# Optimization experiments

Measured on AMD Instinct MI355X. Metric: run time of the kernel, lower is better.

Reference implementation:

```python
import jax, jax.numpy as jnp
import numpy as np

HARDLIM_THRESH = 0.2


def setup_inputs() -> dict:
    key = jax.random.key(0)
    k_inp, k_w1, k_b1, k_w2, k_b2 = jax.random.split(key, 5)
    B, D, H, F = 16384, 4096, 2048, 512
    scale1 = 1.0 / np.sqrt(D)
    scale2 = 1.0 / np.sqrt(H)
    return {
        "inp": jax.random.normal(k_inp, (B, D), dtype=jnp.float32),
        "W1": jax.random.normal(k_w1, (H, D), dtype=jnp.float32) * scale1,
        "b1": jax.random.normal(k_b1, (H,), dtype=jnp.float32) * scale1,
        "W2": jax.random.normal(k_w2, (F, H), dtype=jnp.float32) * scale2,
        "b2": jax.random.normal(k_b2, (F,), dtype=jnp.float32) * scale2,
        "k": 8,
    }


def reference(inp, W1, b1, W2, b2, k):
    # Linear -> ReLU -> Linear
    h = jax.nn.relu(inp @ W1.T + b1)            # [B, H]
    logits = h @ W2.T + b2                      # [B, F]
    # 'hard' attention: sigmoid -> keep top-k (zero the rest) -> hardlim(0.2)
    s = jax.nn.sigmoid(logits)
    topk_vals, _ = jax.lax.top_k(s, k)          # [B, k]
    kth = topk_vals[:, -1:]                     # per-row k-th largest value
    gated = jnp.where(s >= kth, s, 0.0)         # GetTopK: zero non-top-k entries
    out = jnp.where(gated > HARDLIM_THRESH, 1.0, 0.0).astype(inp.dtype)
    return out
```

## Files before the change

kernel.cpp:

```cpp
#include <hip/hip_runtime.h>
#include <math.h>
#include <type_traits>


#define BM 128
#define BN 128
#define BK 16

#define TAU   1.0e-4f
#define L02F -1.3862943611198906f

typedef __attribute__((ext_vector_type(8))) short  bf16x8;
typedef __attribute__((ext_vector_type(8))) ushort u16x8;
typedef __attribute__((ext_vector_type(4))) float  f32x4;

__device__ inline ushort bfhi(float f)   { return (ushort)(__float_as_uint(f) >> 16); }
__device__ inline float  bfhif(float f)  { return __uint_as_float(__float_as_uint(f) & 0xFFFF0000u); }

__device__ inline void gload_lds16(const void* g, void* l) {
    __builtin_amdgcn_global_load_lds(
        (const __attribute__((address_space(1))) unsigned int*)g,
        (__attribute__((address_space(3))) unsigned int*)l, 16, 0, 0);
}

__global__ __launch_bounds__(256) void split_kernel(
    const float* __restrict__ src, ushort* __restrict__ hi,
    ushort* __restrict__ lo, size_t n4)
{
    size_t i = (size_t)blockIdx.x * 256 + threadIdx.x;
    size_t stride = (size_t)gridDim.x * 256;
    for (; i < n4; i += stride) {
        float4 v = ((const float4*)src)[i];
        ushort4 h, l;
        h.x = bfhi(v.x); l.x = bfhi(v.x - bfhif(v.x));
        h.y = bfhi(v.y); l.y = bfhi(v.y - bfhif(v.y));
        h.z = bfhi(v.z); l.z = bfhi(v.z - bfhif(v.z));
        h.w = bfhi(v.w); l.w = bfhi(v.w - bfhif(v.w));
        ((ushort4*)hi)[i] = h;
        ((ushort4*)lo)[i] = l;
    }
}

template<int OUT_SPLIT>
__global__ __launch_bounds__(512, 2) void bgemm_glds(
    const ushort* __restrict__ aH, const ushort* __restrict__ aL,
    const ushort* __restrict__ wH, const ushort* __restrict__ wL,
    const float* __restrict__ bias,
    ushort* __restrict__ Chi, ushort* __restrict__ Clo,
    float* __restrict__ C32,
    int N, int K, int nbm, int nbn)
{
    __shared__ ushort lds[73728];
    const int t    = threadIdx.x;
    const int lane = t & 63;
    const int wave = t >> 6;
    const int wr   = wave >> 1;
    const int wc   = wave & 1;
    const int l15  = lane & 15;
    const int l4   = lane >> 4;

    const int bid = blockIdx.x;
    const int xcd = bid & 7;
    const int j   = bid >> 3;
    const int bm  = xcd * (nbm >> 3) + j / nbn;
    const int bn  = j % nbn;

    const int c   = lane & 3;
    const int rA0 = (wave * 2 + 0) * 16 + (lane >> 2);
    const int rA1 = (wave * 2 + 1) * 16 + (lane >> 2);
    const int rB  = wave * 16 + (lane >> 2);
    const size_t offA0 = (size_t)(bm * 256 + rA0) * K + (size_t)((c ^ ((rA0 >> 1) & 3)) * 8);
    const size_t offA1 = (size_t)(bm * 256 + rA1) * K + (size_t)((c ^ ((rA1 >> 1) & 3)) * 8);
    const size_t offB  = (size_t)(bn * 128 + rB ) * K + (size_t)((c ^ ((rB  >> 1) & 3)) * 8);
    const ushort* sAh0 = aH + offA0; const ushort* sAl0 = aL + offA0;
    const ushort* sAh1 = aH + offA1; const ushort* sAl1 = aL + offA1;
    const ushort* sBh  = wH + offB;  const ushort* sBl  = wL + offB;

    f32x4 acc[4][4];
    #pragma unroll
    for (int mi = 0; mi < 4; ++mi)
        #pragma unroll
        for (int ni = 0; ni < 4; ++ni)
            acc[mi][ni] = (f32x4){0.f, 0.f, 0.f, 0.f};

    auto stage = [&](int b, int kt) {
        const size_t ko = (size_t)kt * 32;
        ushort* L0 = &lds[b * 24576];
        gload_lds16(sAh0 + ko, L0 + (wave * 2 + 0) * 512);
        gload_lds16(sAh1 + ko, L0 + (wave * 2 + 1) * 512);
        gload_lds16(sAl0 + ko, L0 + 8192 + (wave * 2 + 0) * 512);
        gload_lds16(sAl1 + ko, L0 + 8192 + (wave * 2 + 1) * 512);
        gload_lds16(sBh + ko,  L0 + 16384 + wave * 512);
        gload_lds16(sBl + ko,  L0 + 20480 + wave * 512);
    };
    auto frag_read = [&](int b, bf16x8 ah[4], bf16x8 al[4], bf16x8 bh[4], bf16x8 bl[4]) {
        const ushort* L0 = &lds[b * 24576];
        #pragma unroll
        for (int mi = 0; mi < 4; ++mi) {
            int row = wr * 64 + mi * 16 + l15;
            int o = row * 32 + ((l4 ^ ((row >> 1) & 3)) << 3);
            ah[mi] = *(const bf16x8*)&L0[o];
            al[mi] = *(const bf16x8*)&L0[8192 + o];
        }
        #pragma unroll
        for (int ni = 0; ni < 4; ++ni) {
            int row = wc * 64 + ni * 16 + l15;
            int o = row * 32 + ((l4 ^ ((row >> 1) & 3)) << 3);
            bh[ni] = *(const bf16x8*)&L0[16384 + o];
            bl[ni] = *(const bf16x8*)&L0[20480 + o];
        }
    };
    auto do_mfma = [&](bf16x8 ah[4], bf16x8 al[4], bf16x8 bh[4], bf16x8 bl[4]) {
        __builtin_amdgcn_s_setprio(1);
        #pragma unroll
        for (int mi = 0; mi < 4; ++mi)
            #pragma unroll
            for (int ni = 0; ni < 4; ++ni) {
                acc[mi][ni] = __builtin_amdgcn_mfma_f32_16x16x32_bf16(ah[mi], bh[ni], acc[mi][ni], 0, 0, 0);
                acc[mi][ni] = __builtin_amdgcn_mfma_f32_16x16x32_bf16(ah[mi], bl[ni], acc[mi][ni], 0, 0, 0);
                acc[mi][ni] = __builtin_amdgcn_mfma_f32_16x16x32_bf16(al[mi], bh[ni], acc[mi][ni], 0, 0, 0);
            }
        __builtin_amdgcn_s_setprio(0);
    };

    stage(0, 0);
    stage(1, 1);
    asm volatile("s_waitcnt vmcnt(6)");
    __builtin_amdgcn_s_barrier();

    const int nt = K / 32;
    bf16x8 ah[4], al[4], bh[4], bl[4];

    for (int kt = 0; kt < nt - 2; ++kt) {
        frag_read(kt % 3, ah, al, bh, bl);
        stage((kt + 2) % 3, kt + 2);
        __builtin_amdgcn_sched_barrier(0);
        do_mfma(ah, al, bh, bl);
        asm volatile("s_waitcnt vmcnt(6)");
        asm volatile("s_waitcnt lgkmcnt(0)\n\ts_barrier" ::: "memory");
    }
    {
        frag_read((nt - 2) % 3, ah, al, bh, bl);
        do_mfma(ah, al, bh, bl);
        asm volatile("s_waitcnt vmcnt(0)");
        asm volatile("s_waitcnt lgkmcnt(0)\n\ts_barrier" ::: "memory");
    }
    {
        frag_read((nt - 1) % 3, ah, al, bh, bl);
        do_mfma(ah, al, bh, bl);
    }

    #pragma unroll
    for (int ni = 0; ni < 4; ++ni) {
        int col = bn * 128 + wc * 64 + ni * 16 + l15;
        float bv = bias[col];
        #pragma unroll
        for (int mi = 0; mi < 4; ++mi) {
            int rowb = bm * 256 + wr * 64 + mi * 16 + l4 * 4;
            #pragma unroll
            for (int r = 0; r < 4; ++r) {
                float v = acc[mi][ni][r] + bv;
                size_t idx = (size_t)(rowb + r) * N + col;
                if (OUT_SPLIT) {
                    v = fmaxf(v, 0.0f);
                    Chi[idx] = bfhi(v);
                    Clo[idx] = bfhi(v - bfhif(v));
                } else {
                    C32[idx] = v;
                }
            }
        }
    }
}

__global__ __launch_bounds__(512, 2) void bgemm1_8p(
    const float* __restrict__ inp,
    const ushort* __restrict__ w1h, const ushort* __restrict__ w1l,
    const float* __restrict__ b1,
    ushort* __restrict__ Chi, ushort* __restrict__ Clo)
{
    __shared__ ushort lds[73728];
    const int t    = threadIdx.x;
    const int lane = t & 63;
    const int wave = t >> 6;
    const int wr   = wave >> 1;
    const int wc   = wave & 1;
    const int l15  = lane & 15;
    const int l4   = lane >> 4;

    const int bid = blockIdx.x;
    const int xcd = bid & 7;
    const int j   = bid >> 3;
    const int bm  = xcd * 8 + (j >> 4);
    const int bn  = j & 15;

    const int ra  = t >> 1;
    const int kh  = t & 1;
    const int rb  = t >> 2;
    const int kqb = (t & 3) ^ ((rb >> 1) & 3);

    const float*  Abase = inp + ((size_t)(bm * 256 + ra)) * 4096 + kh * 16;
    const ushort* Bsh   = w1h + ((size_t)(bn * 128 + rb)) * 4096 + kqb * 8;
    const ushort* Bsl   = w1l + ((size_t)(bn * 128 + rb)) * 4096 + kqb * 8;

    f32x4 acc[4][4];
    #pragma unroll
    for (int mi = 0; mi < 4; ++mi)
        #pragma unroll
        for (int ni = 0; ni < 4; ++ni)
            acc[mi][ni] = (f32x4){0.f, 0.f, 0.f, 0.f};

    auto a_write = [&](int b, const f32x4 av[4]) {
        ushort h[16], l[16];
        #pragma unroll
        for (int i = 0; i < 4; ++i) {
            #pragma unroll
            for (int jj = 0; jj < 4; ++jj) {
                float x = av[i][jj];
                h[i * 4 + jj] = bfhi(x);
                l[i * 4 + jj] = bfhi(x - bfhif(x));
            }
        }
        ushort* A0 = &lds[b * 24576 + ra * 32];
        #pragma unroll
        for (int jj = 0; jj < 2; ++jj) {
            int u = (((2 * kh + jj) ^ ((ra >> 1) & 3)) << 3);
            *(u16x8*)&A0[u]        = *(const u16x8*)&h[jj * 8];
            *(u16x8*)&A0[8192 + u] = *(const u16x8*)&l[jj * 8];
        }
    };
    auto w_issue = [&](int b, int kt) {
        gload_lds16(Bsh + (size_t)kt * 32, &lds[b * 24576 + 16384 + wave * 512]);
        gload_lds16(Bsl + (size_t)kt * 32, &lds[b * 24576 + 20480 + wave * 512]);
    };
    auto a_load_asm = [&](int kt, f32x4 av[4]) {
        const float* p = Abase + (size_t)kt * 32;
        asm volatile("global_load_dwordx4 %0, %1, off"           : "=v"(av[0]) : "v"(p));
        asm volatile("global_load_dwordx4 %0, %1, off offset:16" : "=v"(av[1]) : "v"(p));
        asm volatile("global_load_dwordx4 %0, %1, off offset:32" : "=v"(av[2]) : "v"(p));
        asm volatile("global_load_dwordx4 %0, %1, off offset:48" : "=v"(av[3]) : "v"(p));
    };
    auto frag_read = [&](int b, bf16x8 ah[4], bf16x8 al[4], bf16x8 bh[4], bf16x8 bl[4]) {
        const ushort* L0 = &lds[b * 24576];
        #pragma unroll
        for (int mi = 0; mi < 4; ++mi) {
            int row = wr * 64 + mi * 16 + l15;
            int o = row * 32 + ((l4 ^ ((row >> 1) & 3)) << 3);
            ah[mi] = *(const bf16x8*)&L0[o];
            al[mi] = *(const bf16x8*)&L0[8192 + o];
        }
        #pragma unroll
        for (int ni = 0; ni < 4; ++ni) {
            int row = wc * 64 + ni * 16 + l15;
            int o = row * 32 + ((l4 ^ ((row >> 1) & 3)) << 3);
            bh[ni] = *(const bf16x8*)&L0[16384 + o];
            bl[ni] = *(const bf16x8*)&L0[20480 + o];
        }
    };
    auto do_mfma = [&](bf16x8 ah[4], bf16x8 al[4], bf16x8 bh[4], bf16x8 bl[4]) {
        __builtin_amdgcn_s_setprio(1);
        #pragma unroll
        for (int mi = 0; mi < 4; ++mi)
            #pragma unroll
            for (int ni = 0; ni < 4; ++ni) {
                acc[mi][ni] = __builtin_amdgcn_mfma_f32_16x16x32_bf16(ah[mi], bh[ni], acc[mi][ni], 0, 0, 0);
                acc[mi][ni] = __builtin_amdgcn_mfma_f32_16x16x32_bf16(ah[mi], bl[ni], acc[mi][ni], 0, 0, 0);
                acc[mi][ni] = __builtin_amdgcn_mfma_f32_16x16x32_bf16(al[mi], bh[ni], acc[mi][ni], 0, 0, 0);
            }
        __builtin_amdgcn_s_setprio(0);
    };
    #define BAR_KEEP() asm volatile("s_waitcnt lgkmcnt(0)\n\ts_barrier" ::: "memory")

    f32x4 avA[4], avB[4];
    {
        f32x4 a0[4];
        #pragma unroll
        for (int i = 0; i < 4; ++i) a0[i] = *(const f32x4*)(Abase + i * 4);
        a_write(0, a0);
        w_issue(0, 0);
        a_load_asm(1, avA);
        __builtin_amdgcn_sched_barrier(0);
        w_issue(1, 1);
        __builtin_amdgcn_sched_barrier(0);
        asm volatile("s_waitcnt vmcnt(6)");
        BAR_KEEP();
    }

    const int nt = 128;
    auto tile_body = [&](int kt, f32x4 (&cons)[4], f32x4 (&prod)[4]) {
        const int cur = kt % 3, nb1 = (kt + 1) % 3, nb2 = (kt + 2) % 3;
        bf16x8 ah[4], al[4], bh[4], bl[4];
        frag_read(cur, ah, al, bh, bl);
        a_load_asm(kt + 2, prod);
        __builtin_amdgcn_sched_barrier(0);
        w_issue(nb2, kt + 2);
        __builtin_amdgcn_sched_barrier(0);
        asm volatile("s_waitcnt vmcnt(6)");
        asm volatile("" : "+v"(cons[0]), "+v"(cons[1]), "+v"(cons[2]), "+v"(cons[3]));
        __builtin_amdgcn_sched_barrier(0);
        a_write(nb1, cons);
        do_mfma(ah, al, bh, bl);
        BAR_KEEP();
    };

    for (int kt = 0; kt < nt - 2; kt += 2) {
        tile_body(kt,     avA, avB);
        tile_body(kt + 1, avB, avA);
    }
    {
        const int kt = nt - 2;
        bf16x8 ah[4], al[4], bh[4], bl[4];
        frag_read(kt % 3, ah, al, bh, bl);
        asm volatile("s_waitcnt vmcnt(0)");
        asm volatile("" : "+v"(avA[0]), "+v"(avA[1]), "+v"(avA[2]), "+v"(avA[3]));
        __builtin_amdgcn_sched_barrier(0);
        a_write((kt + 1) % 3, avA);
        do_mfma(ah, al, bh, bl);
        BAR_KEEP();
    }
    {
        bf16x8 ah[4], al[4], bh[4], bl[4];
        frag_read((nt - 1) % 3, ah, al, bh, bl);
        do_mfma(ah, al, bh, bl);
    }

    #pragma unroll
    for (int ni = 0; ni < 4; ++ni) {
        int col = bn * 128 + wc * 64 + ni * 16 + l15;
        float bv = b1[col];
        #pragma unroll
        for (int mi = 0; mi < 4; ++mi) {
            int rowb = bm * 256 + wr * 64 + mi * 16 + l4 * 4;
            #pragma unroll
            for (int r = 0; r < 4; ++r) {
                float v = fmaxf(acc[mi][ni][r] + bv, 0.0f);
                size_t idx = (size_t)(rowb + r) * 2048 + col;
                Chi[idx] = bfhi(v);
                Clo[idx] = bfhi(v - bfhif(v));
            }
        }
    }
    #undef BAR_KEEP
}

__global__ __launch_bounds__(256) void repair_r1(
    const float* __restrict__ inp,
    const float* __restrict__ W1, const float* __restrict__ b1,
    double* __restrict__ h64,
    const int* __restrict__ risky, const int* __restrict__ cnt, int maxr)
{
    int c = *cnt; if (c > maxr) c = maxr;
    const int by = blockIdx.y;
    if (by * 4 >= c) return;
    __shared__ float Xs[4][4096];
    const int t = threadIdx.x;

    int ridx[4];
    #pragma unroll
    for (int r = 0; r < 4; ++r) {
        int slot = by * 4 + r;
        ridx[r] = risky[slot < c ? slot : (c - 1)];
    }
    #pragma unroll
    for (int i = 0; i < 16; ++i) {
        int lin = t + i * 256;
        int r = lin >> 10, q = lin & 1023;
        *(float4*)&Xs[r][q * 4] = *(const float4*)(inp + (size_t)ridx[r] * 4096 + q * 4);
    }
    __syncthreads();

    const int n0 = blockIdx.x * 512 + t;
    const int n1 = n0 + 256;
    const float* w0 = W1 + (size_t)n0 * 4096;
    const float* w1 = W1 + (size_t)n1 * 4096;
    double acc[2][4] = {};

    for (int k = 0; k < 4096; k += 4) {
        float4 a0 = *(const float4*)(w0 + k);
        float4 a1 = *(const float4*)(w1 + k);
        float xr[4][4];
        #pragma unroll
        for (int r = 0; r < 4; ++r)
            *(float4*)&xr[r][0] = *(const float4*)&Xs[r][k];
        const float* ap0 = &a0.x;
        const float* ap1 = &a1.x;
        #pragma unroll
        for (int j = 0; j < 4; ++j) {
            double wd0 = (double)ap0[j];
            double wd1 = (double)ap1[j];
            #pragma unroll
            for (int r = 0; r < 4; ++r) {
                double xd = (double)xr[r][j];
                acc[0][r] = fma(wd0, xd, acc[0][r]);
                acc[1][r] = fma(wd1, xd, acc[1][r]);
            }
        }
    }

    double bv0 = (double)b1[n0], bv1 = (double)b1[n1];
    #pragma unroll
    for (int r = 0; r < 4; ++r) {
        int slot = by * 4 + r;
        if (slot < c) {
            h64[(size_t)slot * 2048 + n0] = fmax(acc[0][r] + bv0, 0.0);
            h64[(size_t)slot * 2048 + n1] = fmax(acc[1][r] + bv1, 0.0);
        }
    }
}

__global__ __launch_bounds__(256) void repair_r2(
    const double* __restrict__ h64,
    const float* __restrict__ W2, const float* __restrict__ b2,
    double* __restrict__ L64,
    const int* __restrict__ cnt, int maxr)
{
    int c = *cnt; if (c > maxr) c = maxr;
    const int by = blockIdx.y;
    if (by * 4 >= c) return;
    __shared__ double Xs[4][2048];
    const int t = threadIdx.x;

    #pragma unroll
    for (int i = 0; i < 16; ++i) {
        int lin = t + i * 256;
        int r = lin >> 10, q = lin & 1023;
        int slot = by * 4 + r; if (slot >= c) slot = c - 1;
        *(double2*)&Xs[r][q * 2] = *(const double2*)(h64 + (size_t)slot * 2048 + q * 2);
    }
    __syncthreads();

    const int n0 = t;
    const int n1 = t + 256;
    const float* w0 = W2 + (size_t)n0 * 2048;
    const float* w1 = W2 + (size_t)n1 * 2048;
    double acc[2][4] = {};

    for (int k = 0; k < 2048; k += 4) {
        float4 a0 = *(const float4*)(w0 + k);
        float4 a1 = *(const float4*)(w1 + k);
        double xr[4][4];
        #pragma unroll
        for (int r = 0; r < 4; ++r) {
            *(double2*)&xr[r][0] = *(const double2*)&Xs[r][k];
            *(double2*)&xr[r][2] = *(const double2*)&Xs[r][k + 2];
        }
        const float* ap0 = &a0.x;
        const float* ap1 = &a1.x;
        #pragma unroll
        for (int j = 0; j < 4; ++j) {
            double wd0 = (double)ap0[j];
            double wd1 = (double)ap1[j];
            #pragma unroll
            for (int r = 0; r < 4; ++r) {
                acc[0][r] = fma(wd0, xr[r][j], acc[0][r]);
                acc[1][r] = fma(wd1, xr[r][j], acc[1][r]);
            }
        }
    }

    double bv0 = (double)b2[n0], bv1 = (double)b2[n1];
    #pragma unroll
    for (int r = 0; r < 4; ++r) {
        int slot = by * 4 + r;
        if (slot < c) {
            L64[(size_t)slot * 512 + n0] = acc[0][r] + bv0;
            L64[(size_t)slot * 512 + n1] = acc[1][r] + bv1;
        }
    }
}

template<typename TA, int MODE>
__global__ __launch_bounds__(256, 1) void gemm64(
    const TA* __restrict__ A, int lda,
    const float* __restrict__ W, int ldw,
    const float* __restrict__ bias,
    double* __restrict__ out64, int N, int K)
{
    __shared__ double As[BK][BM + 2];
    __shared__ double Bs[BK][BN + 2];
    const int t  = threadIdx.x;
    const int tm = t >> 4;
    const int tn = t & 15;
    const size_t bm = blockIdx.x;
    const size_t bn = blockIdx.y;
    const TA*    Ab = A + bm * BM * (size_t)lda;
    const float* Wb = W + bn * BN * (size_t)ldw;

    double acc[8][8] = {};

    for (int k0 = 0; k0 < K; k0 += BK) {
        #pragma unroll
        for (int i = 0; i < 2; ++i) {
            int f   = t + i * 256;
            int row = f >> 2;
            int kc  = (f & 3) << 2;
            if constexpr (std::is_same<TA, double>::value) {
                double2 v0 = *(const double2*)(Ab + (size_t)row * lda + k0 + kc);
                double2 v1 = *(const double2*)(Ab + (size_t)row * lda + k0 + kc + 2);
                As[kc + 0][row] = v0.x; As[kc + 1][row] = v0.y;
                As[kc + 2][row] = v1.x; As[kc + 3][row] = v1.y;
            } else {
                float4 va = *(const float4*)(Ab + (size_t)row * lda + k0 + kc);
                As[kc + 0][row] = (double)va.x; As[kc + 1][row] = (double)va.y;
                As[kc + 2][row] = (double)va.z; As[kc + 3][row] = (double)va.w;
            }
            float4 vb = *(const float4*)(Wb + (size_t)row * ldw + k0 + kc);
            Bs[kc + 0][row] = (double)vb.x; Bs[kc + 1][row] = (double)vb.y;
            Bs[kc + 2][row] = (double)vb.z; Bs[kc + 3][row] = (double)vb.w;
        }
        __syncthreads();
        #pragma unroll
        for (int k = 0; k < BK; ++k) {
            double a[8], b[8];
            #pragma unroll
            for (int i = 0; i < 4; ++i) {
                *(double2*)&a[i * 2] = *(const double2*)&As[k][tm * 8 + i * 2];
                *(double2*)&b[i * 2] = *(const double2*)&Bs[k][tn * 8 + i * 2];
            }
            #pragma unroll
            for (int i = 0; i < 8; ++i)
                #pragma unroll
                for (int j = 0; j < 8; ++j)
                    acc[i][j] = fma(a[i], b[j], acc[i][j]);
        }
        __syncthreads();
    }

    double bv[8];
    if (MODE != 2) {
        #pragma unroll
        for (int j = 0; j < 8; ++j) bv[j] = (double)bias[bn * BN + tn * 8 + j];
    }

    #pragma unroll
    for (int i = 0; i < 8; ++i) {
        size_t row  = bm * BM + (size_t)tm * 8 + i;
        size_t base = row * (size_t)N + bn * BN + tn * 8;
        #pragma unroll
        for (int j = 0; j < 8; ++j) {
            double v = acc[i][j];
            if (MODE == 0) out64[base + j] = fmax(v + bv[j], 0.0);
            if (MODE == 1) out64[base + j] = v + bv[j];
            if (MODE == 2) out64[base + j] += v;
        }
    }
}

__global__ void init_repair(int* risky, int* cnt, int maxr)
{
    int i = blockIdx.x * 256 + threadIdx.x;
    if (i == 0) *cnt = 0;
    if (i < maxr) risky[i] = 0;
}

__global__ __launch_bounds__(256) void margin_topk32(
    const float* L, float* O, int ncols,
    const int* __restrict__ kp, int* __restrict__ risky, int* __restrict__ cnt,
    int maxr)
{
    const int wave = threadIdx.x >> 6;
    const int lane = threadIdx.x & 63;
    const int k = *kp;
    const size_t row = (size_t)blockIdx.x * 4 + wave;
    const float* Lr = L + row * (size_t)ncols;

    float v[8];
    *(float4*)&v[0] = *(const float4*)(Lr + lane * 8);
    *(float4*)&v[4] = *(const float4*)(Lr + lane * 8 + 4);
    float w[8];
    #pragma unroll
    for (int j = 0; j < 8; ++j) w[j] = v[j];

    float kth = -3.0e38f, minD = 3.0e38f;
    for (int it = 0; it < k; ++it) {
        float mv = w[0]; int mj = 0;
        #pragma unroll
        for (int j = 1; j < 8; ++j)
            if (w[j] > mv) { mv = w[j]; mj = j; }
        int mi = lane * 8 + mj;
        #pragma unroll
        for (int off = 32; off; off >>= 1) {
            float ov = __shfl_xor(mv, off);
            int   oi = __shfl_xor(mi, off);
            if (ov > mv || (ov == mv && oi < mi)) { mv = ov; mi = oi; }
        }
        kth = mv;
        minD = fminf(minD, fabsf(mv - L02F));
        if ((mi >> 3) == lane) w[mi & 7] = -3.0e38f;
    }
    float nv = w[0];
    #pragma unroll
    for (int j = 1; j < 8; ++j) nv = fmaxf(nv, w[j]);
    #pragma unroll
    for (int off = 32; off; off >>= 1) nv = fmaxf(nv, __shfl_xor(nv, off));

    bool risk = ((kth - nv) < 2.0f * TAU) || (minD < TAU);
    if (risk && lane == 0) {
        int p = atomicAdd(cnt, 1);
        if (p < maxr) risky[p] = (int)row;
    }

    float o[8];
    #pragma unroll
    for (int j = 0; j < 8; ++j)
        o[j] = (v[j] >= kth && v[j] > L02F) ? 1.0f : 0.0f;
    float* Op = O + row * (size_t)ncols + lane * 8;
    *(float4*)&Op[0] = *(const float4*)&o[0];
    *(float4*)&Op[4] = *(const float4*)&o[4];
}

__global__ __launch_bounds__(256) void topk64_kernel(
    const double* __restrict__ L, float* __restrict__ O, int ncols,
    const int* __restrict__ kp,
    const int* __restrict__ risky, const int* __restrict__ cnt, int maxr)
{
    const int wave = threadIdx.x >> 6;
    const int lane = threadIdx.x & 63;
    const int k = *kp;
    size_t pos = (size_t)blockIdx.x * 4 + wave;
    size_t row = pos;
    if (cnt) {
        int c = *cnt; if (c > maxr) c = maxr;
        if ((int)pos >= c) return;
        row = (size_t)risky[pos];
    }
    const double* Lr = L + pos * (size_t)ncols;

    double v[8];
    #pragma unroll
    for (int j = 0; j < 8; ++j) {
        double l = Lr[lane * 8 + j];
        v[j] = 1.0 / (1.0 + exp(-l));
    }
    double w[8];
    #pragma unroll
    for (int j = 0; j < 8; ++j) w[j] = v[j];

    double kth = -1.0e300;
    for (int it = 0; it < k; ++it) {
        double mv = w[0]; int mj = 0;
        #pragma unroll
        for (int j = 1; j < 8; ++j)
            if (w[j] > mv) { mv = w[j]; mj = j; }
        int mi = lane * 8 + mj;
        #pragma unroll
        for (int off = 32; off; off >>= 1) {
            double ov = __shfl_xor(mv, off);
            int    oi = __shfl_xor(mi, off);
            if (ov > mv || (ov == mv && oi < mi)) { mv = ov; mi = oi; }
        }
        kth = mv;
        if ((mi >> 3) == lane) w[mi & 7] = -1.0e300;
    }

    float o[8];
    #pragma unroll
    for (int j = 0; j < 8; ++j)
        o[j] = (v[j] >= kth && v[j] > 0.2) ? 1.0f : 0.0f;
    float* Op = O + row * (size_t)ncols + lane * 8;
    *(float4*)&Op[0] = *(const float4*)&o[0];
    *(float4*)&Op[4] = *(const float4*)&o[4];
}

extern "C" void kernel_launch(void* const* d_in, const int* in_sizes, int n_in,
                              void* d_out, int out_size, void* d_ws, size_t ws_size,
                              hipStream_t stream) {
    const float* inp = (const float*)d_in[0];
    const float* W1  = (const float*)d_in[1];
    const float* b1  = (const float*)d_in[2];
    const float* W2  = (const float*)d_in[3];
    const float* b2  = (const float*)d_in[4];
    const int*   kp  = (const int*)d_in[5];

    const int H = in_sizes[2];
    const int F = in_sizes[4];
    const int D = in_sizes[1] / H;
    const int B = in_sizes[0] / D;
    float* out = (float*)d_out;

    const int MAXR = 8192;
    const size_t szHpair = (size_t)B * H * 4;
    const size_t szW1p   = (size_t)H * D * 4;
    const size_t szW2p   = (size_t)F * H * 4;
    const size_t szInpP  = (size_t)B * D * 4;
    const size_t needMain = szHpair + szW1p + szW2p + (size_t)MAXR * 4 + 256;
    const size_t needA    = needMain + szInpP;
    const bool shapeOK = (D == 4096 && H == 2048 && F == 512 && B == 16384);

    if (shapeOK && ws_size >= needMain) {
        ushort* h_hi  = (ushort*)d_ws;
        ushort* h_lo  = h_hi + (size_t)B * H;
        ushort* w1h   = (ushort*)((char*)d_ws + szHpair);
        ushort* w1l   = w1h + (size_t)H * D;
        ushort* w2h   = (ushort*)((char*)d_ws + szHpair + szW1p);
        ushort* w2l   = w2h + (size_t)F * H;
        int*    risky = (int*)((char*)d_ws + szHpair + szW1p + szW2p);
        int*    cnt   = risky + MAXR;
        double* h64   = (double*)d_ws;
        double* L64   = (double*)((char*)d_ws + szHpair);
        float*  l32   = out;

        init_repair<<<(MAXR + 255) / 256, 256, 0, stream>>>(risky, cnt, MAXR);
        split_kernel<<<2048, 256, 0, stream>>>(W1, w1h, w1l, (size_t)H * D / 4);
        split_kernel<<<512, 256, 0, stream>>>(W2, w2h, w2l, (size_t)F * H / 4);

        if (ws_size >= needA) {
            ushort* inH = (ushort*)((char*)d_ws + needMain);
            ushort* inL = inH + (size_t)B * D;
            split_kernel<<<4096, 256, 0, stream>>>(inp, inH, inL, (size_t)B * D / 4);
            bgemm_glds<1><<<1024, 512, 0, stream>>>(
                inH, inL, w1h, w1l, b1, h_hi, h_lo, nullptr, H, D, B / 256, H / 128);
        } else {
            bgemm1_8p<<<1024, 512, 0, stream>>>(inp, w1h, w1l, b1, h_hi, h_lo);
        }
        bgemm_glds<0><<<256, 512, 0, stream>>>(
            h_hi, h_lo, w2h, w2l, b2, nullptr, nullptr, l32, F, H, B / 256, F / 128);

        margin_topk32<<<B / 4, 256, 0, stream>>>(l32, out, F, kp, risky, cnt, MAXR);
        repair_r1<<<dim3(4, MAXR / 4), 256, 0, stream>>>(
            inp, W1, b1, h64, risky, cnt, MAXR);
        repair_r2<<<dim3(1, MAXR / 4), 256, 0, stream>>>(
            h64, W2, b2, L64, cnt, MAXR);
        topk64_kernel<<<MAXR / 4, 256, 0, stream>>>(L64, out, F, kp, risky, cnt, MAXR);
    } else {
        int Hc = H, Bc = 0;
        for (;;) {
            size_t perRow = (size_t)F * 8 + (size_t)Hc * 8;
            Bc = (int)((ws_size / perRow) / BM) * BM;
            if (Bc >= BM || Hc <= BM) break;
            Hc >>= 1;
        }
        if (Bc < BM) Bc = BM;
        if (Bc > B)  Bc = B;
        double* L   = (double*)d_ws;
        double* h64 = L + (size_t)Bc * F;

        for (int b0 = 0; b0 < B; b0 += Bc) {
            int bc = (B - b0 < Bc) ? (B - b0) : Bc;
            for (int h0 = 0; h0 < H; h0 += Hc) {
                int hc = (H - h0 < Hc) ? (H - h0) : Hc;
                gemm64<float, 0><<<dim3(bc / BM, hc / BN), 256, 0, stream>>>(
                    inp + (size_t)b0 * D, D, W1 + (size_t)h0 * D, D, b1 + h0,
                    h64, hc, D);
                if (h0 == 0)
                    gemm64<double, 1><<<dim3(bc / BM, F / BN), 256, 0, stream>>>(
                        h64, hc, W2 + h0, H, b2, L, F, hc);
                else
                    gemm64<double, 2><<<dim3(bc / BM, F / BN), 256, 0, stream>>>(
                        h64, hc, W2 + h0, H, b2, L, F, hc);
            }
            topk64_kernel<<<bc / 4, 256, 0, stream>>>(
                L, out + (size_t)b0 * F, F, kp, nullptr, nullptr, 0);
        }
    }
}
```

Measured before the change: 1.402 ms.

## Use 256x256 tiled pre-split GEMM1, fold counter init, retile repair kernel

Replaces the first GEMM path with a new kernel that loads pre-split bf16 hi/lo operands through direct global-to-LDS loads into 256x256 tiles, double-buffered. Each tile gets more operand reuse and the grid needs fewer blocks. The init_repair launch is dropped and the counter reset moves into the first split kernel, which saves one launch. The repair_r1 kernel now handles 8 rows per block with one output column per thread. The code path now requires enough workspace for a split copy of the input and drops the fallback that split the input on the fly. The double-buffered loop waits on vmcnt(0) every iteration, which may expose load latency.

```diff
diff --git a/kernel.cpp b/kernel.cpp
--- a/kernel.cpp
+++ b/kernel.cpp
@@ -25,8 +25,9 @@
 
 __global__ __launch_bounds__(256) void split_kernel(
     const float* __restrict__ src, ushort* __restrict__ hi,
-    ushort* __restrict__ lo, size_t n4)
-{
+    ushort* __restrict__ lo, size_t n4, int* cnt)
+{
+    if (cnt && blockIdx.x == 0 && threadIdx.x == 0) *cnt = 0;
     size_t i = (size_t)blockIdx.x * 256 + threadIdx.x;
     size_t stride = (size_t)gridDim.x * 256;
     for (; i < n4; i += stride) {
@@ -38,6 +39,121 @@
         h.w = bfhi(v.w); l.w = bfhi(v.w - bfhif(v.w));
         ((ushort4*)hi)[i] = h;
         ((ushort4*)lo)[i] = l;
+    }
+}
+
+__global__ __launch_bounds__(512, 2) void bgemm1_256(
+    const ushort* __restrict__ aH, const ushort* __restrict__ aL,
+    const ushort* __restrict__ wH, const ushort* __restrict__ wL,
+    const float* __restrict__ b1,
+    ushort* __restrict__ Chi, ushort* __restrict__ Clo)
+{
+    __shared__ ushort lds[65536];
+    const int t    = threadIdx.x;
+    const int lane = t & 63;
+    const int wave = t >> 6;
+    const int wr   = wave >> 1;
+    const int wc   = wave & 1;
+    const int l15  = lane & 15;
+    const int l4   = lane >> 4;
+
+    const int bid = blockIdx.x;
+    const int xcd = bid & 7;
+    const int j   = bid >> 3;
+    const int bm  = xcd * 8 + (j >> 3);
+    const int bn  = j & 7;
+
+    const int cq = lane & 3;
+    const int r0 = wave * 32 + (lane >> 2);
+    const int r1 = r0 + 16;
+    const size_t sw0 = (size_t)((cq ^ ((r0 >> 1) & 3)) * 8);
+    const size_t sw1 = (size_t)((cq ^ ((r1 >> 1) & 3)) * 8);
+    const size_t gA0 = (size_t)(bm * 256 + r0) * 4096 + sw0;
+    const size_t gA1 = (size_t)(bm * 256 + r1) * 4096 + sw1;
+    const size_t gB0 = (size_t)(bn * 256 + r0) * 4096 + sw0;
+    const size_t gB1 = (size_t)(bn * 256 + r1) * 4096 + sw1;
+
+    f32x4 acc[4][8];
+    #pragma unroll
+    for (int mi = 0; mi < 4; ++mi)
+        #pragma unroll
+        for (int ni = 0; ni < 8; ++ni)
+            acc[mi][ni] = (f32x4){0.f, 0.f, 0.f, 0.f};
+
+    auto stage = [&](int b, int kt) {
+        const size_t ko = (size_t)kt * 32;
+        ushort* L0 = &lds[b * 32768];
+        gload_lds16(aH + gA0 + ko, L0 + wave * 1024);
+        gload_lds16(aH + gA1 + ko, L0 + wave * 1024 + 512);
+        gload_lds16(aL + gA0 + ko, L0 + 8192 + wave * 1024);
+        gload_lds16(aL + gA1 + ko, L0 + 8192 + wave * 1024 + 512);
+        gload_lds16(wH + gB0 + ko, L0 + 16384 + wave * 1024);
+        gload_lds16(wH + gB1 + ko, L0 + 16384 + wave * 1024 + 512);
+        gload_lds16(wL + gB0 + ko, L0 + 24576 + wave * 1024);
+        gload_lds16(wL + gB1 + ko, L0 + 24576 + wave * 1024 + 512);
+    };
+    auto compute = [&](int b) {
+        const ushort* L0 = &lds[b * 32768];
+        bf16x8 ah[4], al[4];
+        #pragma unroll
+        for (int mi = 0; mi < 4; ++mi) {
+            int row = wr * 64 + mi * 16 + l15;
+            int o = row * 32 + ((l4 ^ ((row >> 1) & 3)) << 3);
+            ah[mi] = *(const bf16x8*)&L0[o];
+            al[mi] = *(const bf16x8*)&L0[8192 + o];
+        }
+        #pragma unroll
+        for (int h = 0; h < 2; ++h) {
+            bf16x8 bh[4], bl[4];
+            #pragma unroll
+            for (int q = 0; q < 4; ++q) {
+                int row = wc * 128 + (h * 4 + q) * 16 + l15;
+                int o = row * 32 + ((l4 ^ ((row >> 1) & 3)) << 3);
+                bh[q] = *(const bf16x8*)&L0[16384 + o];
+                bl[q] = *(const bf16x8*)&L0[24576 + o];
+            }
+            __builtin_amdgcn_s_setprio(1);
+            #pragma unroll
+            for (int mi = 0; mi < 4; ++mi)
+                #pragma unroll
+                for (int q = 0; q < 4; ++q) {
+                    acc[mi][h * 4 + q] = __builtin_amdgcn_mfma_f32_16x16x32_bf16(ah[mi], bh[q], acc[mi][h * 4 + q], 0, 0, 0);
+                    acc[mi][h * 4 + q] = __builtin_amdgcn_mfma_f32_16x16x32_bf16(ah[mi], bl[q], acc[mi][h * 4 + q], 0, 0, 0);
+                    acc[mi][h * 4 + q] = __builtin_amdgcn_mfma_f32_16x16x32_bf16(al[mi], bh[q], acc[mi][h * 4 + q], 0, 0, 0);
+                }
+            __builtin_amdgcn_s_setprio(0);
+        }
+    };
+
+    stage(0, 0);
+    asm volatile("s_waitcnt vmcnt(0)");
+    __builtin_amdgcn_s_barrier();
+
+    const int nt = 128;
+    for (int kt = 0; kt < nt - 1; ++kt) {
+        stage((kt + 1) & 1, kt + 1);
+        __builtin_amdgcn_sched_barrier(0);
+        compute(kt & 1);
+        asm volatile("s_waitcnt vmcnt(0)");
+        asm volatile("s_waitcnt lgkmcnt(0)\n\ts_barrier" ::: "memory");
+    }
+    compute((nt - 1) & 1);
+
+    #pragma unroll
+    for (int ni = 0; ni < 8; ++ni) {
+        int col = bn * 256 + wc * 128 + ni * 16 + l15;
+        float bv = b1[col];
+        #pragma unroll
+        for (int mi = 0; mi < 4; ++mi) {
+            int rowb = bm * 256 + wr * 64 + mi * 16 + l4 * 4;
+            #pragma unroll
+            for (int r = 0; r < 4; ++r) {
+                float v = fmaxf(acc[mi][ni][r] + bv, 0.0f);
+                size_t idx = (size_t)(rowb + r) * 2048 + col;
+                Chi[idx] = bfhi(v);
+                Clo[idx] = bfhi(v - bfhif(v));
+            }
+        }
     }
 }
 
@@ -173,176 +289,6 @@
     }
 }
 
-__global__ __launch_bounds__(512, 2) void bgemm1_8p(
-    const float* __restrict__ inp,
-    const ushort* __restrict__ w1h, const ushort* __restrict__ w1l,
-    const float* __restrict__ b1,
-    ushort* __restrict__ Chi, ushort* __restrict__ Clo)
-{
-    __shared__ ushort lds[73728];
-    const int t    = threadIdx.x;
-    const int lane = t & 63;
-    const int wave = t >> 6;
-    const int wr   = wave >> 1;
-    const int wc   = wave & 1;
-    const int l15  = lane & 15;
-    const int l4   = lane >> 4;
-
-    const int bid = blockIdx.x;
-    const int xcd = bid & 7;
-    const int j   = bid >> 3;
-    const int bm  = xcd * 8 + (j >> 4);
-    const int bn  = j & 15;
-
-    const int ra  = t >> 1;
-    const int kh  = t & 1;
-    const int rb  = t >> 2;
-    const int kqb = (t & 3) ^ ((rb >> 1) & 3);
-
-    const float*  Abase = inp + ((size_t)(bm * 256 + ra)) * 4096 + kh * 16;
-    const ushort* Bsh   = w1h + ((size_t)(bn * 128 + rb)) * 4096 + kqb * 8;
-    const ushort* Bsl   = w1l + ((size_t)(bn * 128 + rb)) * 4096 + kqb * 8;
-
-    f32x4 acc[4][4];
-    #pragma unroll
-    for (int mi = 0; mi < 4; ++mi)
-        #pragma unroll
-        for (int ni = 0; ni < 4; ++ni)
-            acc[mi][ni] = (f32x4){0.f, 0.f, 0.f, 0.f};
-
-    auto a_write = [&](int b, const f32x4 av[4]) {
-        ushort h[16], l[16];
-        #pragma unroll
-        for (int i = 0; i < 4; ++i) {
-            #pragma unroll
-            for (int jj = 0; jj < 4; ++jj) {
-                float x = av[i][jj];
-                h[i * 4 + jj] = bfhi(x);
-                l[i * 4 + jj] = bfhi(x - bfhif(x));
-            }
-        }
-        ushort* A0 = &lds[b * 24576 + ra * 32];
-        #pragma unroll
-        for (int jj = 0; jj < 2; ++jj) {
-            int u = (((2 * kh + jj) ^ ((ra >> 1) & 3)) << 3);
-            *(u16x8*)&A0[u]        = *(const u16x8*)&h[jj * 8];
-            *(u16x8*)&A0[8192 + u] = *(const u16x8*)&l[jj * 8];
-        }
-    };
-    auto w_issue = [&](int b, int kt) {
-        gload_lds16(Bsh + (size_t)kt * 32, &lds[b * 24576 + 16384 + wave * 512]);
-        gload_lds16(Bsl + (size_t)kt * 32, &lds[b * 24576 + 20480 + wave * 512]);
-    };
-    auto a_load_asm = [&](int kt, f32x4 av[4]) {
-        const float* p = Abase + (size_t)kt * 32;
-        asm volatile("global_load_dwordx4 %0, %1, off"           : "=v"(av[0]) : "v"(p));
-        asm volatile("global_load_dwordx4 %0, %1, off offset:16" : "=v"(av[1]) : "v"(p));
-        asm volatile("global_load_dwordx4 %0, %1, off offset:32" : "=v"(av[2]) : "v"(p));
-        asm volatile("global_load_dwordx4 %0, %1, off offset:48" : "=v"(av[3]) : "v"(p));
-    };
-    auto frag_read = [&](int b, bf16x8 ah[4], bf16x8 al[4], bf16x8 bh[4], bf16x8 bl[4]) {
-        const ushort* L0 = &lds[b * 24576];
-        #pragma unroll
-        for (int mi = 0; mi < 4; ++mi) {
-            int row = wr * 64 + mi * 16 + l15;
-            int o = row * 32 + ((l4 ^ ((row >> 1) & 3)) << 3);
-            ah[mi] = *(const bf16x8*)&L0[o];
-            al[mi] = *(const bf16x8*)&L0[8192 + o];
-        }
-        #pragma unroll
-        for (int ni = 0; ni < 4; ++ni) {
-            int row = wc * 64 + ni * 16 + l15;
-            int o = row * 32 + ((l4 ^ ((row >> 1) & 3)) << 3);
-            bh[ni] = *(const bf16x8*)&L0[16384 + o];
-            bl[ni] = *(const bf16x8*)&L0[20480 + o];
-        }
-    };
-    auto do_mfma = [&](bf16x8 ah[4], bf16x8 al[4], bf16x8 bh[4], bf16x8 bl[4]) {
-        __builtin_amdgcn_s_setprio(1);
-        #pragma unroll
-        for (int mi = 0; mi < 4; ++mi)
-            #pragma unroll
-            for (int ni = 0; ni < 4; ++ni) {
-                acc[mi][ni] = __builtin_amdgcn_mfma_f32_16x16x32_bf16(ah[mi], bh[ni], acc[mi][ni], 0, 0, 0);
-                acc[mi][ni] = __builtin_amdgcn_mfma_f32_16x16x32_bf16(ah[mi], bl[ni], acc[mi][ni], 0, 0, 0);
-                acc[mi][ni] = __builtin_amdgcn_mfma_f32_16x16x32_bf16(al[mi], bh[ni], acc[mi][ni], 0, 0, 0);
-            }
-        __builtin_amdgcn_s_setprio(0);
-    };
-    #define BAR_KEEP() asm volatile("s_waitcnt lgkmcnt(0)\n\ts_barrier" ::: "memory")
-
-    f32x4 avA[4], avB[4];
-    {
-        f32x4 a0[4];
-        #pragma unroll
-        for (int i = 0; i < 4; ++i) a0[i] = *(const f32x4*)(Abase + i * 4);
-        a_write(0, a0);
-        w_issue(0, 0);
-        a_load_asm(1, avA);
-        __builtin_amdgcn_sched_barrier(0);
-        w_issue(1, 1);
-        __builtin_amdgcn_sched_barrier(0);
-        asm volatile("s_waitcnt vmcnt(6)");
-        BAR_KEEP();
-    }
-
-    const int nt = 128;
-    auto tile_body = [&](int kt, f32x4 (&cons)[4], f32x4 (&prod)[4]) {
-        const int cur = kt % 3, nb1 = (kt + 1) % 3, nb2 = (kt + 2) % 3;
-        bf16x8 ah[4], al[4], bh[4], bl[4];
-        frag_read(cur, ah, al, bh, bl);
-        a_load_asm(kt + 2, prod);
-        __builtin_amdgcn_sched_barrier(0);
-        w_issue(nb2, kt + 2);
-        __builtin_amdgcn_sched_barrier(0);
-        asm volatile("s_waitcnt vmcnt(6)");
-        asm volatile("" : "+v"(cons[0]), "+v"(cons[1]), "+v"(cons[2]), "+v"(cons[3]));
-        __builtin_amdgcn_sched_barrier(0);
-        a_write(nb1, cons);
-        do_mfma(ah, al, bh, bl);
-        BAR_KEEP();
-    };
-
-    for (int kt = 0; kt < nt - 2; kt += 2) {
-        tile_body(kt,     avA, avB);
-        tile_body(kt + 1, avB, avA);
-    }
-    {
-        const int kt = nt - 2;
-        bf16x8 ah[4], al[4], bh[4], bl[4];
-        frag_read(kt % 3, ah, al, bh, bl);
-        asm volatile("s_waitcnt vmcnt(0)");
-        asm volatile("" : "+v"(avA[0]), "+v"(avA[1]), "+v"(avA[2]), "+v"(avA[3]));
-        __builtin_amdgcn_sched_barrier(0);
-        a_write((kt + 1) % 3, avA);
-        do_mfma(ah, al, bh, bl);
-        BAR_KEEP();
-    }
-    {
-        bf16x8 ah[4], al[4], bh[4], bl[4];
-        frag_read((nt - 1) % 3, ah, al, bh, bl);
-        do_mfma(ah, al, bh, bl);
-    }
-
-    #pragma unroll
-    for (int ni = 0; ni < 4; ++ni) {
-        int col = bn * 128 + wc * 64 + ni * 16 + l15;
-        float bv = b1[col];
-        #pragma unroll
-        for (int mi = 0; mi < 4; ++mi) {
-            int rowb = bm * 256 + wr * 64 + mi * 16 + l4 * 4;
-            #pragma unroll
-            for (int r = 0; r < 4; ++r) {
-                float v = fmaxf(acc[mi][ni][r] + bv, 0.0f);
-                size_t idx = (size_t)(rowb + r) * 2048 + col;
-                Chi[idx] = bfhi(v);
-                Clo[idx] = bfhi(v - bfhif(v));
-            }
-        }
-    }
-    #undef BAR_KEEP
-}
-
 __global__ __launch_bounds__(256) void repair_r1(
     const float* __restrict__ inp,
     const float* __restrict__ W1, const float* __restrict__ b1,
@@ -351,60 +297,50 @@
 {
     int c = *cnt; if (c > maxr) c = maxr;
     const int by = blockIdx.y;
-    if (by * 4 >= c) return;
-    __shared__ float Xs[4][4096];
+    if (by * 8 >= c) return;
+    __shared__ float Xs[8][4096];
     const int t = threadIdx.x;
 
-    int ridx[4];
-    #pragma unroll
-    for (int r = 0; r < 4; ++r) {
-        int slot = by * 4 + r;
+    int ridx[8];
+    #pragma unroll
+    for (int r = 0; r < 8; ++r) {
+        int slot = by * 8 + r;
         ridx[r] = risky[slot < c ? slot : (c - 1)];
     }
     #pragma unroll
-    for (int i = 0; i < 16; ++i) {
+    for (int i = 0; i < 32; ++i) {
         int lin = t + i * 256;
         int r = lin >> 10, q = lin & 1023;
         *(float4*)&Xs[r][q * 4] = *(const float4*)(inp + (size_t)ridx[r] * 4096 + q * 4);
     }
     __syncthreads();
 
-    const int n0 = blockIdx.x * 512 + t;
-    const int n1 = n0 + 256;
+    const int n0 = blockIdx.x * 256 + t;
     const float* w0 = W1 + (size_t)n0 * 4096;
-    const float* w1 = W1 + (size_t)n1 * 4096;
-    double acc[2][4] = {};
+    double acc[8] = {};
 
     for (int k = 0; k < 4096; k += 4) {
         float4 a0 = *(const float4*)(w0 + k);
-        float4 a1 = *(const float4*)(w1 + k);
-        float xr[4][4];
-        #pragma unroll
-        for (int r = 0; r < 4; ++r)
+        float xr[8][4];
+        #pragma unroll
+        for (int r = 0; r < 8; ++r)
             *(float4*)&xr[r][0] = *(const float4*)&Xs[r][k];
         const float* ap0 = &a0.x;
-        const float* ap1 = &a1.x;
         #pragma unroll
         for (int j = 0; j < 4; ++j) {
             double wd0 = (double)ap0[j];
-            double wd1 = (double)ap1[j];
-            #pragma unroll
-            for (int r = 0; r < 4; ++r) {
-                double xd = (double)xr[r][j];
-                acc[0][r] = fma(wd0, xd, acc[0][r]);
-                acc[1][r] = fma(wd1, xd, acc[1][r]);
-            }
-        }
-    }
-
-    double bv0 = (double)b1[n0], bv1 = (double)b1[n1];
-    #pragma unroll
-    for (int r = 0; r < 4; ++r) {
-        int slot = by * 4 + r;
-        if (slot < c) {
-            h64[(size_t)slot * 2048 + n0] = fmax(acc[0][r] + bv0, 0.0);
-            h64[(size_t)slot * 2048 + n1] = fmax(acc[1][r] + bv1, 0.0);
-        }
+            #pragma unroll
+            for (int r = 0; r < 8; ++r)
+                acc[r] = fma(wd0, (double)xr[r][j], acc[r]);
+        }
+    }
+
+    double bv0 = (double)b1[n0];
+    #pragma unroll
+    for (int r = 0; r < 8; ++r) {
+        int slot = by * 8 + r;
+        if (slot < c)
+            h64[(size_t)slot * 2048 + n0] = fmax(acc[r] + bv0, 0.0);
     }
 }
 
@@ -546,13 +482,6 @@
     }
 }
 
-__global__ void init_repair(int* risky, int* cnt, int maxr)
-{
-    int i = blockIdx.x * 256 + threadIdx.x;
-    if (i == 0) *cnt = 0;
-    if (i < maxr) risky[i] = 0;
-}
-
 __global__ __launch_bounds__(256) void margin_topk32(
     const float* L, float* O, int ncols,
     const int* __restrict__ kp, int* __restrict__ risky, int* __restrict__ cnt,
@@ -687,7 +616,7 @@
     const size_t needA    = needMain + szInpP;
     const bool shapeOK = (D == 4096 && H == 2048 && F == 512 && B == 16384);
 
-    if (shapeOK && ws_size >= needMain) {
+    if (shapeOK && ws_size >= needA) {
         ushort* h_hi  = (ushort*)d_ws;
         ushort* h_lo  = h_hi + (size_t)B * H;
         ushort* w1h   = (ushort*)((char*)d_ws + szHpair);
@@ -696,28 +625,20 @@
         ushort* w2l   = w2h + (size_t)F * H;
         int*    risky = (int*)((char*)d_ws + szHpair + szW1p + szW2p);
         int*    cnt   = risky + MAXR;
+        ushort* inH   = (ushort*)((char*)d_ws + needMain);
+        ushort* inL   = inH + (size_t)B * D;
         double* h64   = (double*)d_ws;
         double* L64   = (double*)((char*)d_ws + szHpair);
         float*  l32   = out;
 
-        init_repair<<<(MAXR + 255) / 256, 256, 0, stream>>>(risky, cnt, MAXR);
-        split_kernel<<<2048, 256, 0, stream>>>(W1, w1h, w1l, (size_t)H * D / 4);
-        split_kernel<<<512, 256, 0, stream>>>(W2, w2h, w2l, (size_t)F * H / 4);
-
-        if (ws_size >= needA) {
-            ushort* inH = (ushort*)((char*)d_ws + needMain);
-            ushort* inL = inH + (size_t)B * D;
-            split_kernel<<<4096, 256, 0, stream>>>(inp, inH, inL, (size_t)B * D / 4);
-            bgemm_glds<1><<<1024, 512, 0, stream>>>(
-                inH, inL, w1h, w1l, b1, h_hi, h_lo, nullptr, H, D, B / 256, H / 128);
-        } else {
-            bgemm1_8p<<<1024, 512, 0, stream>>>(inp, w1h, w1l, b1, h_hi, h_lo);
-        }
+        split_kernel<<<2048, 256, 0, stream>>>(W1, w1h, w1l, (size_t)H * D / 4, cnt);
+        split_kernel<<<512, 256, 0, stream>>>(W2, w2h, w2l, (size_t)F * H / 4, nullptr);
+        split_kernel<<<4096, 256, 0, stream>>>(inp, inH, inL, (size_t)B * D / 4, nullptr);
+        bgemm1_256<<<512, 512, 0, stream>>>(inH, inL, w1h, w1l, b1, h_hi, h_lo);
         bgemm_glds<0><<<256, 512, 0, stream>>>(
             h_hi, h_lo, w2h, w2l, b2, nullptr, nullptr, l32, F, H, B / 256, F / 128);
-
         margin_topk32<<<B / 4, 256, 0, stream>>>(l32, out, F, kp, risky, cnt, MAXR);
-        repair_r1<<<dim3(4, MAXR / 4), 256, 0, stream>>>(
+        repair_r1<<<dim3(8, MAXR / 8), 256, 0, stream>>>(
             inp, W1, b1, h64, risky, cnt, MAXR);
         repair_r2<<<dim3(1, MAXR / 4), 256, 0, stream>>>(
             h64, W2, b2, L64, cnt, MAXR);
```

New measurement: 1.237 ms. 11.8% less time.
